# Optimization experiments

Measured on AMD Instinct MI355X. Metric: run time of the kernel, lower is better.

Reference implementation:

```python
import jax, jax.numpy as jnp
import numpy as np

HIDDEN = 128
N_NODES = 50000
N_EDGES = 640000


def setup_inputs() -> dict:
    key = jax.random.key(0)
    k1, k2, k3, k4, k5, k6, k7 = jax.random.split(key, 7)
    z = jax.random.normal(k1, (N_NODES, HIDDEN), dtype=jnp.float32)
    edge_index = jax.random.randint(k2, (2, N_EDGES), 0, N_NODES, dtype=jnp.int64)
    # Linear params (torch default uniform(-1/sqrt(fan_in), 1/sqrt(fan_in)))
    b1 = 1.0 / np.sqrt(2 * HIDDEN)
    W1 = jax.random.uniform(k3, (HIDDEN, 2 * HIDDEN), jnp.float32, -b1, b1)
    bias1 = jax.random.uniform(k4, (HIDDEN,), jnp.float32, -b1, b1)
    b2 = 1.0 / np.sqrt(HIDDEN)
    W2 = jax.random.uniform(k5, (1, HIDDEN), jnp.float32, -b2, b2)
    bias2 = jax.random.uniform(k6, (1,), jnp.float32, -b2, b2)
    return {"z": z, "W1": W1, "bias1": bias1, "W2": W2, "bias2": bias2,
            "edge_index": edge_index}


def reference(z, W1, bias1, W2, bias2, edge_index):
    # Gather endpoint embeddings: [E, H] each
    z_src = z[edge_index[0]]
    z_dst = z[edge_index[1]]
    h = jnp.concatenate([z_src, z_dst], axis=-1)  # [E, 2H]
    h = jax.nn.relu(h @ W1.T + bias1)             # [E, H]
    out = h @ W2.T + bias2                        # [E, 1]
    return out.reshape(-1)
```

## Files before the change

kernel.cpp:

```cpp
#include <hip/hip_runtime.h>
#include <hip/hip_bf16.h>


#define N_NODES 50000
#define N_EDGES 640000
#define H 128

using bf16 = __hip_bfloat16;
typedef __attribute__((ext_vector_type(8))) short short8;
typedef __attribute__((ext_vector_type(4))) float f32x4;

static __device__ __forceinline__ short bfbits(float x) {
  __hip_bfloat16 h = __float2bfloat16(x);
  return *reinterpret_cast<short*>(&h);
}

static __device__ __forceinline__ short8 pack8(float4 a, float4 b) {
  short8 r;
  r[0] = bfbits(a.x); r[1] = bfbits(a.y); r[2] = bfbits(a.z); r[3] = bfbits(a.w);
  r[4] = bfbits(b.x); r[5] = bfbits(b.y); r[6] = bfbits(b.z); r[7] = bfbits(b.w);
  return r;
}

__global__ __launch_bounds__(256) void precompute_uv(
    const float* __restrict__ z, const float* __restrict__ W1,
    bf16* __restrict__ U, bf16* __restrict__ V) {
  const int lane = threadIdx.x & 63;
  const int s = threadIdx.x >> 6;
  const int l15 = lane & 15, quad = lane >> 4;
  const int nodebase = blockIdx.x * 32;

  short8 wf[4][4];
#pragma unroll
  for (int t = 0; t < 4; ++t) {
    const int o = s * 64 + t * 16 + l15;
    const float* wp = W1 + (size_t)(o & (H - 1)) * (2 * H) + (o >> 7) * H + quad * 8;
#pragma unroll
    for (int q = 0; q < 4; ++q) {
      const float4* p = reinterpret_cast<const float4*>(wp + q * 32);
      wf[t][q] = pack8(p[0], p[1]);
    }
  }

  int node[2];
  short8 zf[2][4];
#pragma unroll
  for (int m = 0; m < 2; ++m) {
    node[m] = nodebase + m * 16 + l15;
    const int nodeC = node[m] < N_NODES ? node[m] : N_NODES - 1;
    const float* zp = z + (size_t)nodeC * H + quad * 8;
#pragma unroll
    for (int q = 0; q < 4; ++q) {
      const float4* p = reinterpret_cast<const float4*>(zp + q * 32);
      zf[m][q] = pack8(p[0], p[1]);
    }
  }

  f32x4 acc[2][4] = {};
#pragma unroll
  for (int m = 0; m < 2; ++m)
#pragma unroll
    for (int t = 0; t < 4; ++t)
#pragma unroll
      for (int q = 0; q < 4; ++q)
        acc[m][t] =
            __builtin_amdgcn_mfma_f32_16x16x32_bf16(wf[t][q], zf[m][q], acc[m][t], 0, 0, 0);

#pragma unroll
  for (int m = 0; m < 2; ++m) {
    if (node[m] < N_NODES) {
#pragma unroll
      for (int t = 0; t < 4; ++t) {
        const int o = s * 64 + t * 16 + quad * 4;
        bf16* base = (o < H) ? U : V;
        ushort4 st;
        st.x = (unsigned short)bfbits(acc[m][t][0]);
        st.y = (unsigned short)bfbits(acc[m][t][1]);
        st.z = (unsigned short)bfbits(acc[m][t][2]);
        st.w = (unsigned short)bfbits(acc[m][t][3]);
        *reinterpret_cast<ushort4*>(base + (size_t)node[m] * H + (o & (H - 1))) = st;
      }
    }
  }
}

static __device__ __forceinline__ void acc2(unsigned u, unsigned v,
                                            float b1lo, float b1hi,
                                            float w2lo, float w2hi, float& sum) {
  const float ulo = __uint_as_float(u << 16);
  const float uhi = __uint_as_float(u & 0xffff0000u);
  const float vlo = __uint_as_float(v << 16);
  const float vhi = __uint_as_float(v & 0xffff0000u);
  float h0 = ulo + vlo + b1lo; h0 = fmaxf(h0, 0.f);
  float h1 = uhi + vhi + b1hi; h1 = fmaxf(h1, 0.f);
  sum = fmaf(h0, w2lo, sum);
  sum = fmaf(h1, w2hi, sum);
}

__global__ __launch_bounds__(256, 4) void edge_decode(
    const int* __restrict__ eidx, const bf16* __restrict__ Ub,
    const bf16* __restrict__ Vb, const float* __restrict__ bias1,
    const float* __restrict__ W2, const float* __restrict__ bias2,
    float* __restrict__ out) {
  const int lane = threadIdx.x & 63;
  const int w = blockIdx.x * 4 + (int)(threadIdx.x >> 6);
  const int chunk = w * 64;
  const int e8 = lane & 7;

  float b1r[16], w2r[16];
  const float4* bp = reinterpret_cast<const float4*>(bias1 + e8 * 16);
  const float4* wp = reinterpret_cast<const float4*>(W2 + e8 * 16);
#pragma unroll
  for (int q = 0; q < 4; ++q) {
    const float4 b = bp[q], wv = wp[q];
    b1r[q * 4 + 0] = b.x; b1r[q * 4 + 1] = b.y; b1r[q * 4 + 2] = b.z; b1r[q * 4 + 3] = b.w;
    w2r[q * 4 + 0] = wv.x; w2r[q * 4 + 1] = wv.y; w2r[q * 4 + 2] = wv.z; w2r[q * 4 + 3] = wv.w;
  }
  const float b2 = bias2[0];

  const int src = eidx[chunk + lane];
  const int dst = eidx[N_EDGES + chunk + lane];
  const uint4* U4 = reinterpret_cast<const uint4*>(Ub);
  const uint4* V4 = reinterpret_cast<const uint4*>(Vb);

  float res = 0.f;
#pragma unroll
  for (int half = 0; half < 2; ++half) {
    uint4 ua[4], ub[4], va[4], vb[4];
#pragma unroll
    for (int j = 0; j < 4; ++j) {
      const int i = half * 4 + j;
      const int sl = (lane & 56) + i;
      const int s_i = __shfl(src, sl);
      const int d_i = __shfl(dst, sl);
      const uint4* up = U4 + (size_t)s_i * 16 + e8 * 2;
      const uint4* vp = V4 + (size_t)d_i * 16 + e8 * 2;
      ua[j] = up[0]; ub[j] = up[1];
      va[j] = vp[0]; vb[j] = vp[1];
    }
#pragma unroll
    for (int j = 0; j < 4; ++j) {
      const int i = half * 4 + j;
      float sum = 0.f;
      acc2(ua[j].x, va[j].x, b1r[0],  b1r[1],  w2r[0],  w2r[1],  sum);
      acc2(ua[j].y, va[j].y, b1r[2],  b1r[3],  w2r[2],  w2r[3],  sum);
      acc2(ua[j].z, va[j].z, b1r[4],  b1r[5],  w2r[4],  w2r[5],  sum);
      acc2(ua[j].w, va[j].w, b1r[6],  b1r[7],  w2r[6],  w2r[7],  sum);
      acc2(ub[j].x, vb[j].x, b1r[8],  b1r[9],  w2r[8],  w2r[9],  sum);
      acc2(ub[j].y, vb[j].y, b1r[10], b1r[11], w2r[10], w2r[11], sum);
      acc2(ub[j].z, vb[j].z, b1r[12], b1r[13], w2r[12], w2r[13], sum);
      acc2(ub[j].w, vb[j].w, b1r[14], b1r[15], w2r[14], w2r[15], sum);
      sum += __shfl_xor(sum, 1);
      sum += __shfl_xor(sum, 2);
      sum += __shfl_xor(sum, 4);
      if (e8 == i) res = sum + b2;
    }
  }
  out[chunk + lane] = res;
}

extern "C" void kernel_launch(void* const* d_in, const int* in_sizes, int n_in,
                              void* d_out, int out_size, void* d_ws, size_t ws_size,
                              hipStream_t stream) {
  const float* z     = (const float*)d_in[0];
  const float* W1    = (const float*)d_in[1];
  const float* bias1 = (const float*)d_in[2];
  const float* W2    = (const float*)d_in[3];
  const float* bias2 = (const float*)d_in[4];
  const int*   eidx  = (const int*)d_in[5];
  float* out = (float*)d_out;

  bf16* U = (bf16*)d_ws;
  bf16* V = U + (size_t)N_NODES * H;

  hipLaunchKernelGGL(precompute_uv, dim3((N_NODES + 31) / 32), dim3(256), 0, stream,
                     z, W1, U, V);
  hipLaunchKernelGGL(edge_decode, dim3(N_EDGES / 64 / 4), dim3(256), 0, stream,
                     eidx, U, V, bias1, W2, bias2, out);
}
```

Before: 157.5 us.

## Pre-convert z and W1 to bf16 and stage U/V stores through LDS

Adds a separate kernel that converts z and a reordered W1 to bf16 once, so precompute_uv loads bf16 directly and no longer re-reads and converts W1 in fp32 in every block. The U/V output is staged through a shared-memory tile so each global store is a full 16-byte row segment rather than a scattered 8-byte write. The cost is an extra launch plus a full fp32 read and bf16 write of z before the main kernels, and a larger workspace.

```diff
diff --git a/kernel.cpp b/kernel.cpp
--- a/kernel.cpp
+++ b/kernel.cpp
@@ -22,9 +22,35 @@
   return r;
 }
 
+#define ZUNITS (N_NODES * H / 8)
+#define WUNITS (2 * H * H / 8)
+
+__global__ __launch_bounds__(256) void to_bf16(
+    const float* __restrict__ z, const float* __restrict__ W1,
+    bf16* __restrict__ zb, bf16* __restrict__ Wb) {
+  const int u = blockIdx.x * 256 + threadIdx.x;
+  const float4* src;
+  bf16* dst;
+  if (u < ZUNITS) {
+    src = reinterpret_cast<const float4*>(z) + (size_t)u * 2;
+    dst = zb + (size_t)u * 8;
+  } else if (u < ZUNITS + WUNITS) {
+    const int w = u - ZUNITS;
+    const int o = w >> 4;
+    const int k8 = (w & 15) * 8;
+    src = reinterpret_cast<const float4*>(W1 + (size_t)(o & (H - 1)) * (2 * H) +
+                                          (o >> 7) * H + k8);
+    dst = Wb + (size_t)o * H + k8;
+  } else {
+    return;
+  }
+  *reinterpret_cast<short8*>(dst) = pack8(src[0], src[1]);
+}
+
 __global__ __launch_bounds__(256) void precompute_uv(
-    const float* __restrict__ z, const float* __restrict__ W1,
+    const bf16* __restrict__ zb, const bf16* __restrict__ Wb,
     bf16* __restrict__ U, bf16* __restrict__ V) {
+  __shared__ bf16 tile[32][2 * H + 8];
   const int lane = threadIdx.x & 63;
   const int s = threadIdx.x >> 6;
   const int l15 = lane & 15, quad = lane >> 4;
@@ -34,26 +60,21 @@
 #pragma unroll
   for (int t = 0; t < 4; ++t) {
     const int o = s * 64 + t * 16 + l15;
-    const float* wp = W1 + (size_t)(o & (H - 1)) * (2 * H) + (o >> 7) * H + quad * 8;
-#pragma unroll
-    for (int q = 0; q < 4; ++q) {
-      const float4* p = reinterpret_cast<const float4*>(wp + q * 32);
-      wf[t][q] = pack8(p[0], p[1]);
-    }
-  }
-
+    const bf16* wp = Wb + (size_t)o * H + quad * 8;
+#pragma unroll
+    for (int q = 0; q < 4; ++q)
+      wf[t][q] = *reinterpret_cast<const short8*>(wp + q * 32);
+  }
   int node[2];
   short8 zf[2][4];
 #pragma unroll
   for (int m = 0; m < 2; ++m) {
     node[m] = nodebase + m * 16 + l15;
     const int nodeC = node[m] < N_NODES ? node[m] : N_NODES - 1;
-    const float* zp = z + (size_t)nodeC * H + quad * 8;
-#pragma unroll
-    for (int q = 0; q < 4; ++q) {
-      const float4* p = reinterpret_cast<const float4*>(zp + q * 32);
-      zf[m][q] = pack8(p[0], p[1]);
-    }
+    const bf16* zp = zb + (size_t)nodeC * H + quad * 8;
+#pragma unroll
+    for (int q = 0; q < 4; ++q)
+      zf[m][q] = *reinterpret_cast<const short8*>(zp + q * 32);
   }
 
   f32x4 acc[2][4] = {};
@@ -68,18 +89,31 @@
 
 #pragma unroll
   for (int m = 0; m < 2; ++m) {
-    if (node[m] < N_NODES) {
-#pragma unroll
-      for (int t = 0; t < 4; ++t) {
-        const int o = s * 64 + t * 16 + quad * 4;
-        bf16* base = (o < H) ? U : V;
-        ushort4 st;
-        st.x = (unsigned short)bfbits(acc[m][t][0]);
-        st.y = (unsigned short)bfbits(acc[m][t][1]);
-        st.z = (unsigned short)bfbits(acc[m][t][2]);
-        st.w = (unsigned short)bfbits(acc[m][t][3]);
-        *reinterpret_cast<ushort4*>(base + (size_t)node[m] * H + (o & (H - 1))) = st;
-      }
+    const int nl = m * 16 + l15;
+#pragma unroll
+    for (int t = 0; t < 4; ++t) {
+      const int o = s * 64 + t * 16 + quad * 4;
+      ushort4 st;
+      st.x = (unsigned short)bfbits(acc[m][t][0]);
+      st.y = (unsigned short)bfbits(acc[m][t][1]);
+      st.z = (unsigned short)bfbits(acc[m][t][2]);
+      st.w = (unsigned short)bfbits(acc[m][t][3]);
+      *reinterpret_cast<ushort4*>(&tile[nl][o]) = st;
+    }
+  }
+  __syncthreads();
+
+#pragma unroll
+  for (int half = 0; half < 2; ++half) {
+    bf16* base = half ? V : U;
+#pragma unroll
+    for (int it = 0; it < 2; ++it) {
+      const int nl = s * 8 + it * 4 + (lane >> 4);
+      const int oc = (lane & 15) * 8;
+      const short8 v = *reinterpret_cast<const short8*>(&tile[nl][half * H + oc]);
+      const int n = nodebase + nl;
+      if (n < N_NODES)
+        *reinterpret_cast<short8*>(base + (size_t)n * H + oc) = v;
     }
   }
 }
@@ -170,11 +204,15 @@
   const int*   eidx  = (const int*)d_in[5];
   float* out = (float*)d_out;
 
-  bf16* U = (bf16*)d_ws;
-  bf16* V = U + (size_t)N_NODES * H;
-
+  bf16* U  = (bf16*)d_ws;
+  bf16* V  = U + (size_t)N_NODES * H;
+  bf16* zb = V + (size_t)N_NODES * H;
+  bf16* Wb = zb + (size_t)N_NODES * H;
+
+  hipLaunchKernelGGL(to_bf16, dim3((ZUNITS + WUNITS) / 256), dim3(256), 0, stream,
+                     z, W1, zb, Wb);
   hipLaunchKernelGGL(precompute_uv, dim3((N_NODES + 31) / 32), dim3(256), 0, stream,
-                     z, W1, U, V);
+                     zb, Wb, U, V);
   hipLaunchKernelGGL(edge_decode, dim3(N_EDGES / 64 / 4), dim3(256), 0, stream,
                      eidx, U, V, bias1, W2, bias2, out);
 }
```

New measurement: 143.1 us. 1.1x faster.
